# Kernel tuning notes

Measured on AMD Instinct MI355X. Metric: run time of the kernel, lower is better.

The kernel has to match this reference:

```python
import jax, jax.numpy as jnp
import numpy as np

N_HEADS = 16
HEAD_DIM = 64
D_MODEL = N_HEADS * HEAD_DIM  # 1024


def setup_inputs() -> dict:
    key = jax.random.key(0)
    ks = jax.random.split(key, 6)
    B, S, D = 2, 2048, D_MODEL
    s = 0.02
    return {
        "hidden_states": jax.random.normal(ks[0], (B, S, D), jnp.float32),
        "position_bias": jax.random.normal(ks[1], (1, N_HEADS, S, S), jnp.float32),
        "Wq": jax.random.normal(ks[2], (D, D), jnp.float32) * s,
        "Wk": jax.random.normal(ks[3], (D, D), jnp.float32) * s,
        "Wv": jax.random.normal(ks[4], (D, D), jnp.float32) * s,
        "Wo": jax.random.normal(ks[5], (D, D), jnp.float32) * s,
    }


def reference(hidden_states, position_bias, Wq, Wk, Wv, Wo):
    B, S, D = hidden_states.shape

    def split_heads(x):  # [B,S,D] -> [B,H,S,hd]
        return x.reshape(B, S, N_HEADS, HEAD_DIM).transpose(0, 2, 1, 3)

    q = split_heads(hidden_states @ Wq)
    k = split_heads(hidden_states @ Wk)
    v = split_heads(hidden_states @ Wv)

    # T5 attention: NO 1/sqrt(d) scaling; additive relative-position bias.
    scores = jnp.einsum("bhqd,bhkd->bhqk", q, k) + position_bias
    attn = jax.nn.softmax(scores.astype(jnp.float32), axis=-1).astype(scores.dtype)
    ctx = jnp.einsum("bhqk,bhkd->bhqd", attn, v)
    ctx = ctx.transpose(0, 2, 1, 3).reshape(B, S, D)
    return ctx @ Wo
```

## Files before the change

### kernel.cpp

```cpp
#include <hip/hip_runtime.h>
#include <hip/hip_bf16.h>
#include <stdint.h>

typedef __bf16 bf16_t;
typedef __bf16 bf16x4 __attribute__((ext_vector_type(4)));
typedef __bf16 bf16x8 __attribute__((ext_vector_type(8)));
typedef float  f32x4  __attribute__((ext_vector_type(4)));

#define S_LEN 2048
#define NH    16
#define HD    64
#define DM    1024
#define BATCH 2
#define M_TOT (BATCH * S_LEN)
#define SM_SHIFT 18.0f

__device__ __forceinline__ void gload16(const void* g, void* l) {
    __builtin_amdgcn_global_load_lds(
        (const __attribute__((address_space(1))) unsigned int*)g,
        (__attribute__((address_space(3))) unsigned int*)l, 16, 0, 0);
}

__global__ void convert_h(const float* __restrict__ X, bf16_t* __restrict__ Y, int n) {
    int i = (blockIdx.x * 256 + threadIdx.x) * 4;
    if (i >= n) return;
    float4 v = *(const float4*)(X + i);
    union { bf16_t h[4]; uint2 u; } pk;
    pk.h[0] = (bf16_t)v.x; pk.h[1] = (bf16_t)v.y;
    pk.h[2] = (bf16_t)v.z; pk.h[3] = (bf16_t)v.w;
    *(uint2*)(Y + i) = pk.u;
}

__global__ void convert_transpose_w4(const float* __restrict__ W0, const float* __restrict__ W1,
                                     const float* __restrict__ W2, const float* __restrict__ W3,
                                     bf16_t* __restrict__ D0, bf16_t* __restrict__ D3) {
    __shared__ float tile[32][33];
    const int z = blockIdx.z;
    const float* W = z == 0 ? W0 : z == 1 ? W1 : z == 2 ? W2 : W3;
    bf16_t* Wt = z < 3 ? D0 + (size_t)z * DM * DM : D3;
    const int tid = threadIdx.x;
    const int tx = tid & 31, ty = tid >> 5;
    const int bx = blockIdx.x * 32, by = blockIdx.y * 32;
#pragma unroll
    for (int it = 0; it < 4; ++it)
        tile[ty + it * 8][tx] = W[(size_t)(by + ty + it * 8) * DM + bx + tx];
    __syncthreads();
#pragma unroll
    for (int it = 0; it < 4; ++it)
        Wt[(size_t)(bx + ty + it * 8) * DM + by + tx] = (bf16_t)tile[tx][ty + it * 8];
}

template<int BN, int EPI>
__global__ __launch_bounds__(256)
void gemm_glds(const bf16_t* __restrict__ A, const bf16_t* __restrict__ Bt,
               float* __restrict__ Cf, bf16_t* __restrict__ Qb, bf16_t* __restrict__ Kb,
               bf16_t* __restrict__ Vtb, int M, int N, int K)
{
    constexpr int WN = BN / 2;
    constexpr int NJ = WN / 16;
    constexpr int RB = BN / 32;
    __shared__ bf16_t smem[16640];
    bf16_t* At  = smem;
    bf16_t* Bts = smem + 8192;

    const int tid  = threadIdx.x;
    const int lane = tid & 63;
    const int wave = tid >> 6;
    const int lc = lane & 15;
    const int l4 = lane >> 4;
    const int wr = wave >> 1, wc = wave & 1;
    const int m0 = blockIdx.y * 128;
    const int n0 = blockIdx.x * BN;
    const int srow = tid >> 3;
    const int scol = (tid & 7) * 8;

    f32x4 acc[4][NJ] = {};

    for (int k0 = 0; k0 < K; k0 += 64) {
        __syncthreads();
#pragma unroll
        for (int ro = 0; ro < 4; ++ro)
            gload16(A + (size_t)(m0 + ro * 32 + srow) * K + k0 + scol,
                    At + ro * 2048 + wave * 512);
#pragma unroll
        for (int ro = 0; ro < RB; ++ro)
            gload16(Bt + (size_t)(n0 + ro * 32 + srow) * K + k0 + scol,
                    Bts + ro * 2048 + wave * 512);
        __syncthreads();

        bf16x8 af[2][4], bfr[2][NJ];
#pragma unroll
        for (int kk = 0; kk < 2; ++kk) {
#pragma unroll
            for (int i = 0; i < 4; ++i)
                af[kk][i] = *(const bf16x8*)(At + (wr * 64 + i * 16 + lc) * 64 + kk * 32 + l4 * 8);
#pragma unroll
            for (int j = 0; j < NJ; ++j)
                bfr[kk][j] = *(const bf16x8*)(Bts + (wc * WN + j * 16 + lc) * 64 + kk * 32 + l4 * 8);
        }
#pragma unroll
        for (int kk = 0; kk < 2; ++kk)
#pragma unroll
            for (int i = 0; i < 4; ++i)
#pragma unroll
                for (int j = 0; j < NJ; ++j)
                    acc[i][j] = __builtin_amdgcn_mfma_f32_16x16x32_bf16(af[kk][i], bfr[kk][j], acc[i][j], 0, 0, 0);
    }

    if (EPI == 1) {
#pragma unroll
        for (int i = 0; i < 4; ++i)
#pragma unroll
            for (int j = 0; j < NJ; ++j)
#pragma unroll
                for (int r = 0; r < 4; ++r) {
                    int m = m0 + wr * 64 + i * 16 + l4 * 4 + r;
                    int n = n0 + wc * WN + j * 16 + lc;
                    Cf[(size_t)m * N + n] = acc[i][j][r];
                }
    } else {
        const int sel = n0 >> 10;
        if (sel < 2) {
            bf16_t* Dst = sel == 0 ? Qb : Kb;
#pragma unroll
            for (int i = 0; i < 4; ++i)
#pragma unroll
                for (int j = 0; j < NJ; ++j)
#pragma unroll
                    for (int r = 0; r < 4; ++r) {
                        int m = m0 + wr * 64 + i * 16 + l4 * 4 + r;
                        int n = (n0 & 1023) + wc * WN + j * 16 + lc;
                        int b = m >> 11, s = m & 2047, h = n >> 6, d = n & 63;
                        Dst[(((size_t)(b * NH + h)) * S_LEN + s) * HD + d] = (bf16_t)acc[i][j][r];
                    }
        } else {
            __syncthreads();
            bf16_t* Ct = smem;
#pragma unroll
            for (int i = 0; i < 4; ++i)
#pragma unroll
                for (int j = 0; j < NJ; ++j)
#pragma unroll
                    for (int r = 0; r < 4; ++r) {
                        int ml = wr * 64 + i * 16 + l4 * 4 + r;
                        int nl = wc * WN + j * 16 + lc;
                        Ct[nl * 130 + ml] = (bf16_t)acc[i][j][r];
                    }
            __syncthreads();
            const int rr = tid >> 1, c0 = (tid & 1) * 64;
            const int nn = (n0 - 2048) + rr;
            const int hh = nn >> 6, dd = nn & 63;
            const int bb = m0 >> 11, s0 = m0 & 2047;
            bf16_t* dst = Vtb + (((size_t)(bb * NH + hh)) * HD + dd) * S_LEN + s0 + c0;
            const bf16_t* srcr = Ct + rr * 130 + c0;
#pragma unroll
            for (int u = 0; u < 8; ++u)
                *(uint4*)(dst + u * 8) = *(const uint4*)(srcr + u * 8);
        }
    }
}

__global__ __launch_bounds__(512, 1)
void attn_kernel(const bf16_t* __restrict__ Q, const bf16_t* __restrict__ Kin,
                 const bf16_t* __restrict__ Vt, const float* __restrict__ bias,
                 bf16_t* __restrict__ Ctx)
{
    const int tid  = threadIdx.x;
    const int lane = tid & 63;
    const int wave = tid >> 6;
    const int b    = wave >> 2;
    const int ws   = wave & 3;
    const int lc = lane & 15;
    const int l4 = lane >> 4;

    const int f   = blockIdx.x;
    const int xcd = f & 7;
    const int kk_ = f >> 3;
    const int h   = xcd * 2 + (kk_ >> 4);
    const int qt  = kk_ & 15;
    const int qw  = qt * 128 + ws * 32;

    __shared__ bf16_t Kt[2][2][64 * 64];
    __shared__ bf16_t Vs[2][2][64 * 64];
    __shared__ float  Bs[3][128 * 64];

    const bf16_t* Qg = Q + (size_t)(b * NH + h) * S_LEN * HD;
    const bf16_t* Kg[2]; const bf16_t* Vg[2];
#pragma unroll
    for (int bb = 0; bb < 2; ++bb) {
        Kg[bb] = Kin + (size_t)(bb * NH + h) * S_LEN * HD;
        Vg[bb] = Vt  + (size_t)(bb * NH + h) * HD * S_LEN;
    }
    const float* Bg = bias + (size_t)h * S_LEN * S_LEN;

    bf16x8 qf[2][2];
#pragma unroll
    for (int i = 0; i < 2; ++i)
#pragma unroll
        for (int kk = 0; kk < 2; ++kk)
            qf[i][kk] = *(const bf16x8*)(Qg + (size_t)(qw + i * 16 + lc) * HD + kk * 32 + l4 * 8);

    f32x4 cacc[2][4] = {};
    float lsum[2] = {};

    const int r0   = lane >> 3;
    const int gsrc = (lane & 7) ^ r0;
    const int R    = wave * 8;

    auto stageKV = [&](int t, int pbuf) {
        const int kv0 = t * 64;
        gload16(Kg[0] + (size_t)(kv0 + R + r0) * HD + gsrc * 8, &Kt[0][pbuf][R * 64]);
        gload16(Kg[1] + (size_t)(kv0 + R + r0) * HD + gsrc * 8, &Kt[1][pbuf][R * 64]);
        gload16(Vg[0] + (size_t)(R + r0) * S_LEN + kv0 + gsrc * 8, &Vs[0][pbuf][R * 64]);
        gload16(Vg[1] + (size_t)(R + r0) * S_LEN + kv0 + gsrc * 8, &Vs[1][pbuf][R * 64]);
    };

    const int br4 = lane >> 4;
    const int bcg = lane & 15;
    auto stageB = [&](int t, int slot) {
        const int kv0 = t * 64;
#pragma unroll
        for (int c = 0; c < 4; ++c) {
            const int ql = wave * 16 + c * 4 + br4;
            const int sg = bcg ^ ((c & 1) * 4 + br4);
            gload16(Bg + (size_t)(qt * 128 + ql) * S_LEN + kv0 + sg * 4,
                    (char*)&Bs[slot][0] + (wave * 4 + c) * 1024);
        }
    };

    stageKV(0, 0);
    stageB(0, 0);
    stageB(1, 1);

    for (int t = 0; t < 32; ++t) {
        const int buf   = t & 1;
        const int bslot = t % 3;
        __builtin_amdgcn_sched_barrier(0);
        asm volatile("s_waitcnt lgkmcnt(0)" ::: "memory");
        if (t < 31) {
            asm volatile("s_waitcnt vmcnt(4)" ::: "memory");
        } else {
            asm volatile("s_waitcnt vmcnt(0)" ::: "memory");
        }
        __builtin_amdgcn_s_barrier();
        __builtin_amdgcn_sched_barrier(0);
        if (t < 31) stageKV(t + 1, buf ^ 1);
        if (t < 30) stageB(t + 2, (t + 2) % 3);
        __builtin_amdgcn_sched_barrier(0);

        f32x4 bv[2][4];
        const float* Bbuf = &Bs[bslot][0];
#pragma unroll
        for (int i = 0; i < 2; ++i)
#pragma unroll
            for (int j = 0; j < 4; ++j) {
                const int ql = ws * 32 + i * 16 + lc;
                bv[i][j] = *(const f32x4*)(Bbuf + ql * 64 + (((4 * j + l4) ^ (lc & 7)) * 4));
            }

        f32x4 saT[4][2] = {};
        __builtin_amdgcn_s_setprio(1);
#pragma unroll
        for (int kk = 0; kk < 2; ++kk) {
            bf16x8 kf[4];
#pragma unroll
            for (int j = 0; j < 4; ++j)
                kf[j] = *(const bf16x8*)(&Kt[b][buf][(j * 16 + lc) * 64 + (((kk * 4 + l4) ^ (lc & 7)) * 8)]);
#pragma unroll
            for (int j = 0; j < 4; ++j)
#pragma unroll
                for (int i = 0; i < 2; ++i)
                    saT[j][i] = __builtin_amdgcn_mfma_f32_16x16x32_bf16(kf[j], qf[i][kk], saT[j][i], 0, 0, 0);
        }
        __builtin_amdgcn_s_setprio(0);

        union { uint32_t d[4]; bf16x8 v; } pa[2][2];
#pragma unroll
        for (int i = 0; i < 2; ++i) {
            f32x4 pe[4];
#pragma unroll
            for (int j = 0; j < 4; ++j) {
                f32x4 s = (saT[j][i] - SM_SHIFT) + bv[i][j];
                pe[j].x = __expf(s.x); pe[j].y = __expf(s.y);
                pe[j].z = __expf(s.z); pe[j].w = __expf(s.w);
                lsum[i] += (pe[j].x + pe[j].y) + (pe[j].z + pe[j].w);
            }
#pragma unroll
            for (int ks = 0; ks < 2; ++ks) {
                asm("v_cvt_pk_bf16_f32 %0, %1, %2" : "=v"(pa[i][ks].d[0]) : "v"(pe[2*ks].x),   "v"(pe[2*ks].y));
                asm("v_cvt_pk_bf16_f32 %0, %1, %2" : "=v"(pa[i][ks].d[1]) : "v"(pe[2*ks].z),   "v"(pe[2*ks].w));
                asm("v_cvt_pk_bf16_f32 %0, %1, %2" : "=v"(pa[i][ks].d[2]) : "v"(pe[2*ks+1].x), "v"(pe[2*ks+1].y));
                asm("v_cvt_pk_bf16_f32 %0, %1, %2" : "=v"(pa[i][ks].d[3]) : "v"(pe[2*ks+1].z), "v"(pe[2*ks+1].w));
            }
        }

        __builtin_amdgcn_s_setprio(1);
#pragma unroll
        for (int ks = 0; ks < 2; ++ks) {
#pragma unroll
            for (int jd = 0; jd < 4; ++jd) {
                union { bf16x4 h[2]; bf16x8 v; } vv;
                const int row = jd * 16 + lc;
                vv.h[0] = *(const bf16x4*)(&Vs[b][buf][row * 64 + (((4 * ks +     (l4 >> 1)) ^ (lc & 7)) * 8) + 4 * (l4 & 1)]);
                vv.h[1] = *(const bf16x4*)(&Vs[b][buf][row * 64 + (((4 * ks + 2 + (l4 >> 1)) ^ (lc & 7)) * 8) + 4 * (l4 & 1)]);
#pragma unroll
                for (int i = 0; i < 2; ++i)
                    cacc[i][jd] = __builtin_amdgcn_mfma_f32_16x16x32_bf16(pa[i][ks].v, vv.v, cacc[i][jd], 0, 0, 0);
            }
        }
        __builtin_amdgcn_s_setprio(0);
    }

#pragma unroll
    for (int i = 0; i < 2; ++i) {
        lsum[i] += __shfl_xor(lsum[i], 16, 64);
        lsum[i] += __shfl_xor(lsum[i], 32, 64);
    }
    float rinv[2][4];
#pragma unroll
    for (int i = 0; i < 2; ++i)
#pragma unroll
        for (int r = 0; r < 4; ++r)
            rinv[i][r] = 1.0f / __shfl(lsum[i], l4 * 4 + r, 16);

    bf16_t* Co = Ctx + (size_t)b * S_LEN * DM + (size_t)h * HD;
#pragma unroll
    for (int i = 0; i < 2; ++i)
#pragma unroll
        for (int r = 0; r < 4; ++r) {
            int qrow = qw + i * 16 + l4 * 4 + r;
#pragma unroll
            for (int jd = 0; jd < 4; ++jd)
                Co[(size_t)qrow * DM + jd * 16 + lc] = (bf16_t)(cacc[i][jd][r] * rinv[i][r]);
        }
}

extern "C" void kernel_launch(void* const* d_in, const int* in_sizes, int n_in,
                              void* d_out, int out_size, void* d_ws, size_t ws_size,
                              hipStream_t stream)
{
    (void)in_sizes; (void)n_in; (void)out_size; (void)ws_size;
    const float* hs   = (const float*)d_in[0];
    const float* bias = (const float*)d_in[1];
    const float* Wq   = (const float*)d_in[2];
    const float* Wk   = (const float*)d_in[3];
    const float* Wv   = (const float*)d_in[4];
    const float* Wo   = (const float*)d_in[5];
    float* out = (float*)d_out;

    char* ws = (char*)d_ws;
    bf16_t* Hbf   = (bf16_t*)(ws);
    bf16_t* Wqkvt = (bf16_t*)(ws + ( 8u << 20));
    bf16_t* Wot   = (bf16_t*)(ws + (14u << 20));
    bf16_t* Qb    = (bf16_t*)(ws + (16u << 20));
    bf16_t* Kb    = (bf16_t*)(ws + (24u << 20));
    bf16_t* Vtb   = (bf16_t*)(ws + (32u << 20));
    bf16_t* Ctx   = (bf16_t*)(ws + (40u << 20));

    convert_h<<<4096, 256, 0, stream>>>(hs, Hbf, M_TOT * DM);
    dim3 tg(32, 32, 4);
    convert_transpose_w4<<<tg, 256, 0, stream>>>(Wq, Wk, Wv, Wo, Wqkvt, Wot);

    dim3 gq(3 * DM / 128, M_TOT / 128);
    gemm_glds<128, 0><<<gq, 256, 0, stream>>>(Hbf, Wqkvt, nullptr, Qb, Kb, Vtb,
                                              M_TOT, 3 * DM, DM);

    attn_kernel<<<256, 512, 0, stream>>>(Qb, Kb, Vtb, bias, Ctx);

    dim3 go(DM / 64, M_TOT / 128);
    gemm_glds<64, 1><<<go, 256, 0, stream>>>(Ctx, Wot, out, nullptr, nullptr, nullptr,
                                             M_TOT, DM, DM);
}
```

Before: 181.9 us.

## Stage position bias through registers as bf16 in LDS with 128-wide tiles

```diff
diff --git a/kernel.cpp b/kernel.cpp
--- a/kernel.cpp
+++ b/kernel.cpp
@@ -182,7 +182,7 @@
 
     __shared__ bf16_t Kt[2][2][64 * 64];
     __shared__ bf16_t Vs[2][2][64 * 64];
-    __shared__ float  Bs[3][128 * 64];
+    __shared__ bf16_t Bs[2][128 * 128];
 
     const bf16_t* Qg = Q + (size_t)(b * NH + h) * S_LEN * HD;
     const bf16_t* Kg[2]; const bf16_t* Vg[2];
@@ -215,47 +215,67 @@
         gload16(Vg[1] + (size_t)(R + r0) * S_LEN + kv0 + gsrc * 8, &Vs[1][pbuf][R * 64]);
     };
 
-    const int br4 = lane >> 4;
-    const int bcg = lane & 15;
-    auto stageB = [&](int t, int slot) {
-        const int kv0 = t * 64;
-#pragma unroll
-        for (int c = 0; c < 4; ++c) {
-            const int ql = wave * 16 + c * 4 + br4;
-            const int sg = bcg ^ ((c & 1) * 4 + br4);
-            gload16(Bg + (size_t)(qt * 128 + ql) * S_LEN + kv0 + sg * 4,
-                    (char*)&Bs[slot][0] + (wave * 4 + c) * 1024);
+    const int brow = lane >> 5;
+    const int bcol = lane & 31;
+    uint4 breg[8];
+    auto bload = [&](int s) {
+#pragma unroll
+        for (int c = 0; c < 8; ++c) {
+            const int r = wave * 16 + 2 * c + brow;
+            breg[c] = *(const uint4*)(Bg + (size_t)(qt * 128 + r) * S_LEN + s * 128 + bcol * 4);
         }
     };
+    auto bwrite = [&](int slot) {
+#pragma unroll
+        for (int c = 0; c < 8; ++c) {
+            const int r = wave * 16 + 2 * c + brow;
+            const float* fp = (const float*)&breg[c];
+            bf16x4 hv = {(bf16_t)fp[0], (bf16_t)fp[1], (bf16_t)fp[2], (bf16_t)fp[3]};
+            *(bf16x4*)(&Bs[slot][r * 128 + ((bcol ^ (r & 15)) * 4)]) = hv;
+        }
+    };
 
     stageKV(0, 0);
-    stageB(0, 0);
-    stageB(1, 1);
+    __builtin_amdgcn_sched_barrier(0);
+    bload(0);
+    bwrite(0);
+    asm volatile("s_waitcnt lgkmcnt(0)" ::: "memory");
+    __builtin_amdgcn_s_barrier();
 
     for (int t = 0; t < 32; ++t) {
-        const int buf   = t & 1;
-        const int bslot = t % 3;
+        const int buf  = t & 1;
+        const int p    = t & 1;
+        const int slot = (t >> 1) & 1;
+        if (t > 0) {
+            __builtin_amdgcn_sched_barrier(0);
+            asm volatile("s_waitcnt lgkmcnt(0)" ::: "memory");
+            if ((t & 1) && t <= 29) {
+                asm volatile("s_waitcnt vmcnt(8)" ::: "memory");
+            } else {
+                asm volatile("s_waitcnt vmcnt(0)" ::: "memory");
+            }
+            __builtin_amdgcn_s_barrier();
+            __builtin_amdgcn_sched_barrier(0);
+        }
+        if (t < 31) stageKV(t + 1, buf ^ 1);
         __builtin_amdgcn_sched_barrier(0);
-        asm volatile("s_waitcnt lgkmcnt(0)" ::: "memory");
-        if (t < 31) {
-            asm volatile("s_waitcnt vmcnt(4)" ::: "memory");
+        if (!(t & 1)) {
+            if ((t >> 1) + 1 <= 15) bload((t >> 1) + 1);
         } else {
-            asm volatile("s_waitcnt vmcnt(0)" ::: "memory");
-        }
-        __builtin_amdgcn_s_barrier();
+            if ((t >> 1) + 1 <= 15) bwrite(slot ^ 1);
+        }
         __builtin_amdgcn_sched_barrier(0);
-        if (t < 31) stageKV(t + 1, buf ^ 1);
-        if (t < 30) stageB(t + 2, (t + 2) % 3);
-        __builtin_amdgcn_sched_barrier(0);
 
         f32x4 bv[2][4];
-        const float* Bbuf = &Bs[bslot][0];
 #pragma unroll
         for (int i = 0; i < 2; ++i)
 #pragma unroll
             for (int j = 0; j < 4; ++j) {
-                const int ql = ws * 32 + i * 16 + lc;
-                bv[i][j] = *(const f32x4*)(Bbuf + ql * 64 + (((4 * j + l4) ^ (lc & 7)) * 4));
+                const int q = ws * 32 + i * 16 + lc;
+                const int g = p * 16 + j * 4 + l4;
+                bf16x4 hb = *(const bf16x4*)(&Bs[slot][q * 128 + ((g ^ lc) * 4)]);
+                bv[i][j].x = (float)hb.x; bv[i][j].y = (float)hb.y;
+                bv[i][j].z = (float)hb.z; bv[i][j].w = (float)hb.w;
             }
 
         f32x4 saT[4][2] = {};
```

Measured after the change: 181.5 us. About the same (-0.2%).
